# Kernel optimization log

Measured on AMD Instinct MI355X. Metric: run time of the kernel, lower is better.

Reference implementation:

```python
import jax, jax.numpy as jnp
import numpy as np

L, C, H, FF = 12, 768, 12, 3072
DH = C // H
VOCAB = 30522
B, P, T = 64, 196, 40
PATCH_FLAT = 768  # 16*16*3
MAXP, MAXW = P + 1, T + 2


def _ln(x, w, b, eps):
    m = jnp.mean(x, axis=-1, keepdims=True)
    v = jnp.mean(jnp.square(x - m), axis=-1, keepdims=True)
    return (x - m) * jax.lax.rsqrt(v + eps) * w + b


def setup_inputs() -> dict:
    key = jax.random.key(0)
    ks = iter(jax.random.split(key, 40))
    s = 0.02
    rn = lambda shape: jax.random.normal(next(ks), shape, jnp.float32) * s
    return {
        'vis_in': jax.random.normal(next(ks), (B, P, PATCH_FLAT), jnp.float32),
        'txt_in': jax.random.randint(next(ks), (B, T), 0, VOCAB),
        'vis_mask': jnp.ones((B, P), jnp.int32),
        'txt_mask': jnp.ones((B, T), jnp.int32),
        'patch_w': rn((C, PATCH_FLAT)), 'patch_b': jnp.zeros((C,), jnp.float32),
        'w_embed': rn((VOCAB, C)),
        't_pos': rn((MAXW, C)),
        'v_pos': rn((1, MAXP, C)),
        'v_cls': rn((1, 1, C)),
        'v_mod': rn((1, 1, C)), 't_mod': rn((1, 1, C)),
        'vn_w': jnp.ones((C,), jnp.float32), 'vn_b': jnp.zeros((C,), jnp.float32),
        'tn_w': jnp.ones((C,), jnp.float32), 'tn_b': jnp.zeros((C,), jnp.float32),
        'qkv_w': rn((L, 3 * C, C)), 'qkv_b': jnp.zeros((L, 3 * C), jnp.float32),
        'proj_w': rn((L, C, C)), 'proj_b': jnp.zeros((L, C), jnp.float32),
        'n1_w': jnp.ones((L, C), jnp.float32), 'n1_b': jnp.zeros((L, C), jnp.float32),
        'n2_w': jnp.ones((L, C), jnp.float32), 'n2_b': jnp.zeros((L, C), jnp.float32),
        'fc1_w': rn((L, FF, C)), 'fc1_b': jnp.zeros((L, FF), jnp.float32),
        'fc2_w': rn((L, C, FF)), 'fc2_b': jnp.zeros((L, C), jnp.float32),
    }


def reference(vis_in, txt_in, vis_mask, txt_mask, patch_w, patch_b, w_embed, t_pos,
              v_pos, v_cls, v_mod, t_mod, vn_w, vn_b, tn_w, tn_b, qkv_w, qkv_b,
              proj_w, proj_b, n1_w, n1_b, n2_w, n2_b, fc1_w, fc1_b, fc2_w, fc2_b):
    Bsz = vis_in.shape[0]
    # patch projection and word embedding
    v_emb = vis_in @ patch_w.T + patch_b                      # [B, P, C]
    t_emb = w_embed[txt_in]                                    # [B, T, C]
    v_emb = jnp.concatenate([jnp.broadcast_to(v_cls, (Bsz, 1, C)), v_emb], axis=1)
    VL = v_emb.shape[1]                                        # P + 1
    v_emb = _ln(v_emb + v_pos[:, :VL] + v_mod, vn_w, vn_b, 1e-5)
    t_emb = _ln(t_emb + t_pos[:T] + t_mod, tn_w, tn_b, 1e-5)
    x = jnp.concatenate([t_emb, v_emb], axis=1)                # [B, N, C], N = T+1+P
    m = jnp.concatenate([txt_mask, jnp.ones((Bsz, 1), txt_mask.dtype), vis_mask], axis=-1)
    # pairwise mask: attn_mask[b,i,j] == 0 -> masked (broadcast over heads)
    masked = (m[:, None, :, None] * m[:, None, None, :]) == 0  # [B,1,N,N]
    scale = DH ** -0.5
    for l in range(L):
        h = _ln(x, n1_w[l], n1_b[l], 1e-6)
        qkv = (h @ qkv_w[l].T + qkv_b[l]).reshape(Bsz, -1, 3, H, DH)
        q = jnp.transpose(qkv[:, :, 0], (0, 2, 1, 3))          # [B,H,N,DH]
        k = jnp.transpose(qkv[:, :, 1], (0, 2, 1, 3))
        v = jnp.transpose(qkv[:, :, 2], (0, 2, 1, 3))
        attn = jnp.einsum('bhqd,bhkd->bhqk', q, k) * scale
        attn = jnp.where(masked, jnp.asarray(-1e30, attn.dtype), attn)
        attn = jax.nn.softmax(attn, axis=-1)
        o = jnp.einsum('bhqk,bhkd->bhqd', attn, v)
        o = jnp.transpose(o, (0, 2, 1, 3)).reshape(Bsz, -1, C)
        x = x + (o @ proj_w[l].T + proj_b[l])
        h2 = _ln(x, n2_w[l], n2_b[l], 1e-6)
        h2 = jax.nn.gelu(h2 @ fc1_w[l].T + fc1_b[l], approximate=False)
        x = x + (h2 @ fc2_w[l].T + fc2_b[l])
    return x
```

## Files before the change

kernel.cpp:

```cpp
#include <hip/hip_runtime.h>
#include <hip/hip_bf16.h>

using bf16 = __hip_bfloat16;
typedef __bf16 bfv8 __attribute__((ext_vector_type(8)));
typedef float f32x4 __attribute__((ext_vector_type(4)));

#define DEVI __device__ __forceinline__

constexpr int L_ = 12, C_ = 768, H_ = 12, FF_ = 3072, DH_ = 64;
constexpr int B_ = 64, P_ = 196, T_ = 40;
constexpr int N_ = T_ + 1 + P_;
constexpr int M_ = B_ * N_;
constexpr int MPAD = 15360;
constexpr int NKV = 256;
constexpr int BP_ = B_ * P_;

constexpr size_t OFF_X   = 0;
constexpr size_t SZ_X    = (size_t)MPAD * C_ * 4;
constexpr size_t OFF_H   = OFF_X + SZ_X;
constexpr size_t SZ_H    = (size_t)MPAD * C_ * 2;
constexpr size_t OFF_Q   = OFF_H + SZ_H;
constexpr size_t SZ_QKV1 = (size_t)B_ * H_ * NKV * DH_ * 2;
constexpr size_t OFF_K   = OFF_Q + SZ_QKV1;
constexpr size_t OFF_V   = OFF_K + SZ_QKV1;
constexpr size_t OFF_O   = OFF_V + SZ_QKV1;
constexpr size_t SZ_O    = SZ_H;
constexpr size_t OFF_FFH = OFF_O + SZ_O;
constexpr size_t SZ_FFH  = (size_t)MPAD * FF_ * 2;
constexpr size_t OFF_WB  = OFF_FFH + SZ_FFH;
constexpr size_t SZ_WB   = (size_t)(2304 + 768 + 3072 + 3072) * 768 * 2;
constexpr size_t WS_NEED = OFF_WB + SZ_WB;
constexpr size_t OFF_PTMP = OFF_FFH;
constexpr size_t OFF_VISB = OFF_FFH + (size_t)40 * 1024 * 1024;
constexpr size_t OFF_PWB  = OFF_WB;

DEVI void gld_lds16(const bf16* g, bf16* l) {
  __builtin_amdgcn_global_load_lds((__attribute__((address_space(1))) void*)(g),
                                   (__attribute__((address_space(3))) void*)(l), 16, 0, 0);
}

DEVI void swz_tiles(int bid, int G, int NTC, int& bm, int& bn) {
  const int qq = G >> 3, rr = G & 7;
  const int xcd = bid & 7, base = bid >> 3;
  const int lin = (xcd < rr ? xcd * (qq + 1) : rr * (qq + 1) + (xcd - rr) * qq) + base;
  bm = lin / NTC;
  bn = lin - bm * NTC;
}

DEVI uint packbf(float lo, float hi) {
  union { struct { bf16 x, y; } h; uint u; } r;
  r.h.x = __float2bfloat16(lo); r.h.y = __float2bfloat16(hi);
  return r.u;
}

DEVI float gelu_f(float v) {
  const float p = v * (1.5957691f + 0.07135481f * v * v) * 1.442695041f;
  const float d = exp2f(-p);
  return v / (1.f + d);
}

template <int EPI>
__global__ __launch_bounds__(512, 2) void gemm3s(
    const bf16* __restrict__ A, const bf16* __restrict__ W,
    const float* __restrict__ bias, float* __restrict__ outf,
    float* __restrict__ outf2, bf16* __restrict__ outb,
    bf16* __restrict__ qb, bf16* __restrict__ kb, bf16* __restrict__ vb,
    int Nout, int K, int Mvalid, int NTC) {
  extern __shared__ __align__(16) char lds[];
  constexpr int SLOT = 49152;
  constexpr int BOFF = 32768;

  const int tid = threadIdx.x, wid = tid >> 6, lane = tid & 63;
  const int wm = wid >> 1, wn = wid & 1;
  int bm, bn;
  swz_tiles(blockIdx.x, gridDim.x, NTC, bm, bn);
  const size_t arow0 = (size_t)bm * 256;
  const size_t brow0 = (size_t)bn * 128;

  const int xr = ((lane & 7) ^ (lane >> 3)) * 8;
  const size_t aoff0 = (arow0 + (size_t)wid * 32 + (lane >> 3)) * K + xr;
  const size_t boff0 = (brow0 + (size_t)wid * 16 + (lane >> 3)) * K + xr;

  f32x4 acc[4][4];
#pragma unroll
  for (int m = 0; m < 4; m++)
#pragma unroll
    for (int n = 0; n < 4; n++) acc[m][n] = (f32x4){0.f, 0.f, 0.f, 0.f};

  auto STAGE = [&](int t, int so) {
    char* slot = lds + so;
    const bf16* Ag = A + aoff0 + (size_t)t * 64;
#pragma unroll
    for (int i = 0; i < 4; i++)
      gld_lds16(Ag + (size_t)i * 8 * K, (bf16*)(slot + (wid * 32 + i * 8) * 128));
    const bf16* Wg = W + boff0 + (size_t)t * 64;
#pragma unroll
    for (int i = 0; i < 2; i++)
      gld_lds16(Wg + (size_t)i * 8 * K, (bf16*)(slot + BOFF + (wid * 16 + i * 8) * 128));
  };

  const int la = lane & 15, g = lane >> 4;
  auto COMPUTE = [&](int so) {
    const char* slot = lds + so;
#pragma unroll
    for (int ks = 0; ks < 2; ks++) {
      bfv8 bfr[4];
#pragma unroll
      for (int n = 0; n < 4; n++) {
        const int r = wn * 64 + n * 16 + la;
        bfr[n] = *(const bfv8*)(slot + BOFF + r * 128 + (((ks * 4 + g) ^ (r & 7)) * 16));
      }
#pragma unroll
      for (int m = 0; m < 4; m++) {
        const int r = wm * 64 + m * 16 + la;
        bfv8 af = *(const bfv8*)(slot + r * 128 + (((ks * 4 + g) ^ (r & 7)) * 16));
#pragma unroll
        for (int n = 0; n < 4; n++)
          acc[m][n] = __builtin_amdgcn_mfma_f32_16x16x32_bf16(af, bfr[n], acc[m][n], 0, 0, 0);
      }
    }
  };

  const int NT = K >> 6;
  STAGE(0, 0);
  STAGE(1, SLOT);
  int cs = 0, sp = 2 * SLOT;
  for (int t = 0; t < NT; ++t) {
    if (t + 2 < NT) {
      STAGE(t + 2, sp);
      sp = (sp == 2 * SLOT) ? 0 : sp + SLOT;
      asm volatile("s_waitcnt vmcnt(12)" ::: "memory");
    } else if (t + 1 < NT) {
      asm volatile("s_waitcnt vmcnt(6)" ::: "memory");
    } else {
      asm volatile("s_waitcnt vmcnt(0)" ::: "memory");
    }
    asm volatile("s_barrier" ::: "memory");
    COMPUTE(cs);
    cs = (cs == 2 * SLOT) ? 0 : cs + SLOT;
    asm volatile("s_barrier" ::: "memory");
  }

  const int row0 = (int)arow0 + wm * 64;
  const int col0 = (int)brow0 + wn * 64;
  float bv[4];
#pragma unroll
  for (int n = 0; n < 4; n++) bv[n] = bias[col0 + n * 16 + la];

  if constexpr (EPI == 0 || EPI == 2 || EPI == 4) {
#pragma unroll
    for (int n = 0; n < 4; n++) {
      const int colb = col0 + n * 16 + la;
#pragma unroll
      for (int m = 0; m < 4; m++)
#pragma unroll
        for (int j = 0; j < 4; j++) {
          const int row = row0 + m * 16 + g * 4 + j;
          const float v = acc[m][n][j] + bv[n];
          if constexpr (EPI == 0) outf[(size_t)row * Nout + colb] = v;
          else if constexpr (EPI == 2) outf[(size_t)row * Nout + colb] += v;
          else { if (row < Mvalid) outf2[(size_t)row * Nout + colb] = outf[(size_t)row * Nout + colb] + v; }
        }
    }
  } else if constexpr (EPI == 3) {
#pragma unroll
    for (int m = 0; m < 4; m++)
#pragma unroll
      for (int j = 0; j < 4; j++) {
        const int row = row0 + m * 16 + g * 4 + j;
#pragma unroll
        for (int n = 0; n < 4; n++) {
          const float v = gelu_f(acc[m][n][j] + bv[n]);
          const float p = __shfl_xor(v, 1);
          if (!(lane & 1))
            *(uint*)(outb + (size_t)row * Nout + col0 + n * 16 + la) = packbf(v, p);
        }
      }
  } else {
#pragma unroll
    for (int m = 0; m < 4; m++)
#pragma unroll
      for (int j = 0; j < 4; j++) {
        const int row = row0 + m * 16 + g * 4 + j;
        const bool ok = row < Mvalid;
        const int bI = row / N_;
        const int nI = row - bI * N_;
#pragma unroll
        for (int n = 0; n < 4; n++) {
          const int colb = col0 + n * 16 + la;
          const float v = acc[m][n][j] + bv[n];
          const float p = __shfl_xor(v, 1);
          if (ok && !(lane & 1)) {
            const int s = colb / C_;
            const int rem = colb - s * C_;
            const int hh = rem >> 6, dd = rem & 63;
            bf16* dst = (s == 0) ? qb : (s == 1) ? kb : vb;
            *(uint*)(dst + (((size_t)bI * H_ + hh) * NKV + nI) * DH_ + dd) = packbf(v, p);
          }
        }
      }
  }
}

__global__ __launch_bounds__(256) void conv_weights_k(
    const float* __restrict__ wq, const float* __restrict__ wp,
    const float* __restrict__ wf1, const float* __restrict__ wf2,
    bf16* __restrict__ dst) {
  const long n0 = 2304L * 768 / 4, n1 = 768L * 768 / 4;
  const long n2 = 3072L * 768 / 4;
  const long tot = n0 + n1 + 2 * n2;
  for (long i = (long)blockIdx.x * 256 + threadIdx.x; i < tot; i += (long)gridDim.x * 256) {
    const float* s; long off;
    if (i < n0) { s = wq; off = i; }
    else if (i < n0 + n1) { s = wp; off = i - n0; }
    else if (i < n0 + n1 + n2) { s = wf1; off = i - n0 - n1; }
    else { s = wf2; off = i - n0 - n1 - n2; }
    float4 v = ((const float4*)s)[off];
    union { short4 q; bf16 h[4]; } u;
    u.h[0] = __float2bfloat16(v.x); u.h[1] = __float2bfloat16(v.y);
    u.h[2] = __float2bfloat16(v.z); u.h[3] = __float2bfloat16(v.w);
    ((short4*)dst)[i] = u.q;
  }
}

__global__ __launch_bounds__(256) void f32_to_bf16_k(const float* __restrict__ s,
                                                     bf16* __restrict__ d, long n4) {
  long i = (long)blockIdx.x * 256 + threadIdx.x;
  long stride = (long)gridDim.x * 256;
  for (; i < n4; i += stride) {
    float4 v = ((const float4*)s)[i];
    union { short4 q; bf16 h[4]; } u;
    u.h[0] = __float2bfloat16(v.x); u.h[1] = __float2bfloat16(v.y);
    u.h[2] = __float2bfloat16(v.z); u.h[3] = __float2bfloat16(v.w);
    ((short4*)d)[i] = u.q;
  }
}

__global__ __launch_bounds__(256) void embed_kernel(
    const float* __restrict__ ptmp, const int* __restrict__ txt_in,
    const float* __restrict__ wemb, const float* __restrict__ tpos,
    const float* __restrict__ vpos, const float* __restrict__ vcls,
    const float* __restrict__ vmod, const float* __restrict__ tmod,
    const float* __restrict__ vnw, const float* __restrict__ vnb,
    const float* __restrict__ tnw, const float* __restrict__ tnb,
    float* __restrict__ x) {
  const int row = blockIdx.x;
  const int tid = threadIdx.x;
  if (row >= M_) {
    for (int i = tid; i < C_; i += 256) x[(size_t)row * C_ + i] = 0.f;
    return;
  }
  const int b = row / N_, n = row - (row / N_) * N_;
  const bool istxt = n < T_;
  float e[3];
#pragma unroll
  for (int i = 0; i < 3; i++) {
    const int c = tid + i * 256;
    float v;
    if (istxt) {
      v = wemb[(size_t)txt_in[b * T_ + n] * C_ + c] + tpos[n * C_ + c] + tmod[c];
    } else {
      const int vi = n - T_;
      const float base = (vi == 0) ? vcls[c] : ptmp[((size_t)b * P_ + (vi - 1)) * C_ + c];
      v = base + vpos[vi * C_ + c] + vmod[c];
    }
    e[i] = v;
  }
  float s = e[0] + e[1] + e[2];
  float s2 = e[0] * e[0] + e[1] * e[1] + e[2] * e[2];
#pragma unroll
  for (int d = 1; d < 64; d <<= 1) { s += __shfl_xor(s, d); s2 += __shfl_xor(s2, d); }
  __shared__ float rs[4], rs2[4];
  const int wid = tid >> 6, lane = tid & 63;
  if (lane == 0) { rs[wid] = s; rs2[wid] = s2; }
  __syncthreads();
  s = rs[0] + rs[1] + rs[2] + rs[3];
  s2 = rs2[0] + rs2[1] + rs2[2] + rs2[3];
  const float mean = s * (1.f / C_);
  const float var = s2 * (1.f / C_) - mean * mean;
  const float rr = rsqrtf(var + 1e-5f);
  const float* w = istxt ? tnw : vnw;
  const float* bb = istxt ? tnb : vnb;
#pragma unroll
  for (int i = 0; i < 3; i++) {
    const int c = tid + i * 256;
    x[(size_t)row * C_ + c] = (e[i] - mean) * rr * w[c] + bb[c];
  }
}

__global__ __launch_bounds__(256) void ln_rows(const float* __restrict__ x,
                                               const float* __restrict__ w,
                                               const float* __restrict__ b,
                                               bf16* __restrict__ out, float eps) {
  const int row = blockIdx.x * 4 + (threadIdx.x >> 6);
  const int lane = threadIdx.x & 63;
  if (row >= MPAD) return;
  bf16* op = out + (size_t)row * C_;
  if (row >= M_) {
#pragma unroll
    for (int i = 0; i < 3; i++)
      *(short4*)(op + (lane + 64 * i) * 4) = make_short4(0, 0, 0, 0);
    return;
  }
  const float4* xp = (const float4*)(x + (size_t)row * C_);
  float4 v[3];
  float s = 0.f, s2 = 0.f;
#pragma unroll
  for (int i = 0; i < 3; i++) {
    v[i] = xp[lane + 64 * i];
    s += v[i].x + v[i].y + v[i].z + v[i].w;
    s2 += v[i].x * v[i].x + v[i].y * v[i].y + v[i].z * v[i].z + v[i].w * v[i].w;
  }
#pragma unroll
  for (int d = 1; d < 64; d <<= 1) { s += __shfl_xor(s, d); s2 += __shfl_xor(s2, d); }
  const float mean = s * (1.f / C_);
  const float rr = rsqrtf(s2 * (1.f / C_) - mean * mean + eps);
#pragma unroll
  for (int i = 0; i < 3; i++) {
    const int c0 = (lane + 64 * i) * 4;
    const float4 w4 = *(const float4*)(w + c0);
    const float4 b4 = *(const float4*)(b + c0);
    union { short4 s4; bf16 h[4]; } u;
    u.h[0] = __float2bfloat16((v[i].x - mean) * rr * w4.x + b4.x);
    u.h[1] = __float2bfloat16((v[i].y - mean) * rr * w4.y + b4.y);
    u.h[2] = __float2bfloat16((v[i].z - mean) * rr * w4.z + b4.z);
    u.h[3] = __float2bfloat16((v[i].w - mean) * rr * w4.w + b4.w);
    *(short4*)(op + c0) = u.s4;
  }
}

DEVI float maskval(const int* __restrict__ tm, const int* __restrict__ vm, int b, int j) {
  if (j < T_) return tm[b * T_ + j] ? 1.f : 0.f;
  if (j == T_) return 1.f;
  if (j < N_) return vm[b * P_ + (j - T_ - 1)] ? 1.f : 0.f;
  return 0.f;
}

__global__ __launch_bounds__(256) void attn_fused(
    const bf16* __restrict__ qb, const bf16* __restrict__ kb,
    const bf16* __restrict__ vb, const int* __restrict__ txt_mask,
    const int* __restrict__ vis_mask, bf16* __restrict__ ob) {
  __shared__ alignas(16) __bf16 Vt[64 * 264];
  __shared__ alignas(16) __bf16 Ps[64 * 264];
  const int qblk = blockIdx.x;
  const int bh = blockIdx.y;
  const int b = bh / H_, hh = bh - b * H_;
  const int tid = threadIdx.x, wid = tid >> 6, lane = tid & 63;

  const __bf16* Vg = (const __bf16*)(vb + (size_t)bh * NKV * DH_);
#pragma unroll
  for (int it = 0; it < 8; it++) {
    const int r = lane + 64 * (it & 3);
    const int c8 = (wid + 4 * (it >> 2)) * 8;
    bfv8 v;
    if (r < N_) v = *(const bfv8*)(Vg + (size_t)r * DH_ + c8);
    else { union { int4 i; bfv8 x; } z; z.i = make_int4(0,0,0,0); v = z.x; }
#pragma unroll
    for (int d = 0; d < 8; d++) Vt[(c8 + d) * 264 + r] = v[d];
  }

  const int qbase = qblk * 64 + wid * 16;
  const __bf16* Qg = (const __bf16*)(qb + (size_t)bh * NKV * DH_);
  const __bf16* Kg = (const __bf16*)(kb + (size_t)bh * NKV * DH_);
  bfv8 aq[2];
#pragma unroll
  for (int kk = 0; kk < 2; kk++)
    aq[kk] = *(const bfv8*)(Qg + (size_t)(qbase + (lane & 15)) * DH_ + kk * 32 + (lane >> 4) * 8);

  f32x4 acc[16];
#pragma unroll
  for (int f = 0; f < 16; f++) acc[f] = (f32x4){0.f, 0.f, 0.f, 0.f};
#pragma unroll
  for (int f = 0; f < 16; f++) {
#pragma unroll
    for (int kk = 0; kk < 2; kk++) {
      bfv8 bk = *(const bfv8*)(Kg + (size_t)(f * 16 + (lane & 15)) * DH_ + kk * 32 + (lane >> 4) * 8);
      acc[f] = __builtin_amdgcn_mfma_f32_16x16x32_bf16(aq[kk], bk, acc[f], 0, 0, 0);
    }
  }

  float cm[16];
#pragma unroll
  for (int f = 0; f < 16; f++)
    cm[f] = maskval(txt_mask, vis_mask, b, f * 16 + (lane & 15));

  const float scale = 0.125f;
#pragma unroll
  for (int j = 0; j < 4; j++) {
    const int qr = qbase + (lane >> 4) * 4 + j;
    const float qm = (qr < N_) ? maskval(txt_mask, vis_mask, b, qr) : 1.f;
    float sv[16];
    float mx = -3.0e38f;
#pragma unroll
    for (int f = 0; f < 16; f++) {
      const int col = f * 16 + (lane & 15);
      float sc;
      if (col >= N_) sc = -INFINITY;
      else if (qm * cm[f] == 0.f) sc = -1e30f;
      else sc = acc[f][j] * scale;
      sv[f] = sc;
      mx = fmaxf(mx, sc);
    }
#pragma unroll
    for (int d = 1; d < 16; d <<= 1) mx = fmaxf(mx, __shfl_xor(mx, d));
    float sum = 0.f;
#pragma unroll
    for (int f = 0; f < 16; f++) { const float p = expf(sv[f] - mx); sv[f] = p; sum += p; }
#pragma unroll
    for (int d = 1; d < 16; d <<= 1) sum += __shfl_xor(sum, d);
    const float inv = 1.f / sum;
    const int ql = wid * 16 + (lane >> 4) * 4 + j;
#pragma unroll
    for (int f = 0; f < 16; f++)
      Ps[ql * 264 + f * 16 + (lane & 15)] = (__bf16)(sv[f] * inv);
  }

  __syncthreads();

  f32x4 oacc[4];
#pragma unroll
  for (int n = 0; n < 4; n++) oacc[n] = (f32x4){0.f, 0.f, 0.f, 0.f};
#pragma unroll
  for (int kk = 0; kk < 8; kk++) {
    bfv8 ap = *(const bfv8*)&Ps[(wid * 16 + (lane & 15)) * 264 + kk * 32 + (lane >> 4) * 8];
#pragma unroll
    for (int n = 0; n < 4; n++) {
      bfv8 bv = *(const bfv8*)&Vt[(n * 16 + (lane & 15)) * 264 + kk * 32 + (lane >> 4) * 8];
      oacc[n] = __builtin_amdgcn_mfma_f32_16x16x32_bf16(ap, bv, oacc[n], 0, 0, 0);
    }
  }
#pragma unroll
  for (int n = 0; n < 4; n++)
#pragma unroll
    for (int j = 0; j < 4; j++) {
      const int q = qbase + (lane >> 4) * 4 + j;
      if (q < N_)
        ob[((size_t)b * N_ + q) * C_ + hh * 64 + n * 16 + (lane & 15)] =
            __float2bfloat16(oacc[n][j]);
    }
}

extern "C" void kernel_launch(void* const* d_in, const int* in_sizes, int n_in,
                              void* d_out, int out_size, void* d_ws, size_t ws_size,
                              hipStream_t stream) {
  const float* vis_in  = (const float*)d_in[0];
  const int*   txt_in  = (const int*)d_in[1];
  const int*   vis_mask = (const int*)d_in[2];
  const int*   txt_mask = (const int*)d_in[3];
  const float* patch_w = (const float*)d_in[4];
  const float* patch_b = (const float*)d_in[5];
  const float* w_embed = (const float*)d_in[6];
  const float* t_pos   = (const float*)d_in[7];
  const float* v_pos   = (const float*)d_in[8];
  const float* v_cls   = (const float*)d_in[9];
  const float* v_mod   = (const float*)d_in[10];
  const float* t_mod   = (const float*)d_in[11];
  const float* vn_w = (const float*)d_in[12];
  const float* vn_b = (const float*)d_in[13];
  const float* tn_w = (const float*)d_in[14];
  const float* tn_b = (const float*)d_in[15];
  const float* qkv_w = (const float*)d_in[16];
  const float* qkv_b = (const float*)d_in[17];
  const float* proj_w = (const float*)d_in[18];
  const float* proj_b = (const float*)d_in[19];
  const float* n1_w = (const float*)d_in[20];
  const float* n1_b = (const float*)d_in[21];
  const float* n2_w = (const float*)d_in[22];
  const float* n2_b = (const float*)d_in[23];
  const float* fc1_w = (const float*)d_in[24];
  const float* fc1_b = (const float*)d_in[25];
  const float* fc2_w = (const float*)d_in[26];
  const float* fc2_b = (const float*)d_in[27];

  char* ws = (char*)d_ws;
  if (ws_size < WS_NEED) {
    hipMemsetAsync(d_out, 0, (size_t)out_size * 4, stream);
    return;
  }
  float* x    = (float*)(ws + OFF_X);
  bf16* h     = (bf16*)(ws + OFF_H);
  bf16* qbuf  = (bf16*)(ws + OFF_Q);
  bf16* kbuf  = (bf16*)(ws + OFF_K);
  bf16* vbuf  = (bf16*)(ws + OFF_V);
  bf16* obuf  = (bf16*)(ws + OFF_O);
  bf16* ffh   = (bf16*)(ws + OFF_FFH);
  bf16* wq    = (bf16*)(ws + OFF_WB);
  bf16* wp    = wq + (size_t)2304 * 768;
  bf16* wf1   = wp + (size_t)768 * 768;
  bf16* wf2   = wf1 + (size_t)3072 * 768;
  float* ptmp = (float*)(ws + OFF_PTMP);
  bf16* visb  = (bf16*)(ws + OFF_VISB);
  bf16* pwb   = (bf16*)(ws + OFF_PWB);

  constexpr int LDS3 = 3 * 49152;
  (void)hipFuncSetAttribute((const void*)gemm3s<0>, hipFuncAttributeMaxDynamicSharedMemorySize, LDS3);
  (void)hipFuncSetAttribute((const void*)gemm3s<1>, hipFuncAttributeMaxDynamicSharedMemorySize, LDS3);
  (void)hipFuncSetAttribute((const void*)gemm3s<2>, hipFuncAttributeMaxDynamicSharedMemorySize, LDS3);
  (void)hipFuncSetAttribute((const void*)gemm3s<3>, hipFuncAttributeMaxDynamicSharedMemorySize, LDS3);
  (void)hipFuncSetAttribute((const void*)gemm3s<4>, hipFuncAttributeMaxDynamicSharedMemorySize, LDS3);

  f32_to_bf16_k<<<1024, 256, 0, stream>>>(vis_in, visb, (long)BP_ * C_ / 4);
  f32_to_bf16_k<<<256, 256, 0, stream>>>(patch_w, pwb, (long)C_ * C_ / 4);
  gemm3s<0><<<(BP_ / 256) * (C_ / 128), 512, LDS3, stream>>>(
      visb, pwb, patch_b, ptmp, nullptr, nullptr, nullptr, nullptr, nullptr,
      C_, C_, BP_, C_ / 128);
  embed_kernel<<<MPAD, 256, 0, stream>>>(ptmp, txt_in, w_embed, t_pos, v_pos, v_cls,
                                         v_mod, t_mod, vn_w, vn_b, tn_w, tn_b, x);

  for (int l = 0; l < L_; l++) {
    conv_weights_k<<<2048, 256, 0, stream>>>(
        qkv_w + (size_t)l * 2304 * 768, proj_w + (size_t)l * 768 * 768,
        fc1_w + (size_t)l * 3072 * 768, fc2_w + (size_t)l * 768 * 3072, wq);

    ln_rows<<<MPAD / 4, 256, 0, stream>>>(x, n1_w + l * C_, n1_b + l * C_, h, 1e-6f);
    gemm3s<1><<<(MPAD / 256) * (2304 / 128), 512, LDS3, stream>>>(
        h, wq, qkv_b + (size_t)l * 2304, nullptr, nullptr, nullptr, qbuf, kbuf, vbuf,
        2304, C_, M_, 2304 / 128);
    attn_fused<<<dim3(4, B_ * H_), 256, 0, stream>>>(qbuf, kbuf, vbuf, txt_mask,
                                                     vis_mask, obuf);
    gemm3s<2><<<(MPAD / 256) * (C_ / 128), 512, LDS3, stream>>>(
        obuf, wp, proj_b + (size_t)l * C_, x, nullptr, nullptr, nullptr, nullptr,
        nullptr, C_, C_, M_, C_ / 128);
    ln_rows<<<MPAD / 4, 256, 0, stream>>>(x, n2_w + l * C_, n2_b + l * C_, h, 1e-6f);
    gemm3s<3><<<(MPAD / 256) * (FF_ / 128), 512, LDS3, stream>>>(
        h, wf1, fc1_b + (size_t)l * FF_, nullptr, nullptr, ffh, nullptr, nullptr,
        nullptr, FF_, C_, M_, FF_ / 128);
    if (l < L_ - 1) {
      gemm3s<2><<<(MPAD / 256) * (C_ / 128), 512, LDS3, stream>>>(
          ffh, wf2, fc2_b + (size_t)l * C_, x, nullptr, nullptr, nullptr, nullptr,
          nullptr, C_, FF_, M_, C_ / 128);
    } else {
      gemm3s<4><<<(MPAD / 256) * (C_ / 128), 512, LDS3, stream>>>(
          ffh, wf2, fc2_b + (size_t)l * C_, x, (float*)d_out, nullptr, nullptr,
          nullptr, nullptr, C_, FF_, M_, C_ / 128);
    }
  }
}
```

Baseline: 6.728 ms.

## Restructure GEMM main loop into interleaved two-phase load/MFMA schedule with priority

The GEMM inner loop is split into two half-phases. Each phase loads its LDS fragments into registers, issues part of the next tile's global-to-LDS prefetch, then runs a batch of MFMAs under raised wave priority (s_setprio). The intent is to interleave memory traffic with matrix math across waves, in the style of ping-pong scheduling, rather than staging a whole tile and then computing. Launch bounds drop to one block per CU, which frees registers for the preloaded A fragments but gives up the possibility of two resident blocks. Three LDS slots of 48KB each already exceed what two blocks could share, so occupancy may be unchanged in practice.

```diff
diff --git a/kernel.cpp b/kernel.cpp
--- a/kernel.cpp
+++ b/kernel.cpp
@@ -60,7 +60,7 @@
 }
 
 template <int EPI>
-__global__ __launch_bounds__(512, 2) void gemm3s(
+__global__ __launch_bounds__(512, 1) void gemm8p(
     const bf16* __restrict__ A, const bf16* __restrict__ W,
     const float* __restrict__ bias, float* __restrict__ outf,
     float* __restrict__ outf2, bf16* __restrict__ outb,
@@ -87,58 +87,91 @@
 #pragma unroll
     for (int n = 0; n < 4; n++) acc[m][n] = (f32x4){0.f, 0.f, 0.f, 0.f};
 
-  auto STAGE = [&](int t, int so) {
-    char* slot = lds + so;
+  auto STGa = [&](int t, int so) {
     const bf16* Ag = A + aoff0 + (size_t)t * 64;
-#pragma unroll
-    for (int i = 0; i < 4; i++)
-      gld_lds16(Ag + (size_t)i * 8 * K, (bf16*)(slot + (wid * 32 + i * 8) * 128));
+    char* s = lds + so;
+#pragma unroll
+    for (int i = 0; i < 3; i++)
+      gld_lds16(Ag + (size_t)i * 8 * K, (bf16*)(s + (wid * 32 + i * 8) * 128));
+  };
+  auto STGb = [&](int t, int so) {
+    const bf16* Ag = A + aoff0 + (size_t)t * 64;
     const bf16* Wg = W + boff0 + (size_t)t * 64;
+    char* s = lds + so;
+    gld_lds16(Ag + (size_t)24 * K, (bf16*)(s + (wid * 32 + 24) * 128));
 #pragma unroll
     for (int i = 0; i < 2; i++)
-      gld_lds16(Wg + (size_t)i * 8 * K, (bf16*)(slot + BOFF + (wid * 16 + i * 8) * 128));
+      gld_lds16(Wg + (size_t)i * 8 * K, (bf16*)(s + BOFF + (wid * 16 + i * 8) * 128));
   };
 
   const int la = lane & 15, g = lane >> 4;
-  auto COMPUTE = [&](int so) {
-    const char* slot = lds + so;
-#pragma unroll
-    for (int ks = 0; ks < 2; ks++) {
-      bfv8 bfr[4];
-#pragma unroll
-      for (int n = 0; n < 4; n++) {
+
+  const int NT = K >> 6;
+  STGa(0, 0); STGb(0, 0);
+  STGa(1, SLOT); STGb(1, SLOT);
+  asm volatile("s_waitcnt vmcnt(6)" ::: "memory");
+  __builtin_amdgcn_s_barrier();
+
+  int cs = 0;
+  for (int t = 0; t < NT; ++t) {
+    const int so = cs;
+    int sn = cs + 2 * SLOT; if (sn >= 3 * SLOT) sn -= 3 * SLOT;
+    const char* sa = lds + so;
+    const bool pf = (t + 2 < NT);
+
+    bfv8 af[8], bf0[4];
+#pragma unroll
+    for (int m = 0; m < 4; m++)
+#pragma unroll
+      for (int ks = 0; ks < 2; ks++) {
+        const int r = wm * 64 + m * 16 + la;
+        af[m * 2 + ks] = *(const bfv8*)(sa + r * 128 + (((ks * 4 + g) ^ (r & 7)) * 16));
+      }
+#pragma unroll
+    for (int n = 0; n < 2; n++)
+#pragma unroll
+      for (int ks = 0; ks < 2; ks++) {
         const int r = wn * 64 + n * 16 + la;
-        bfr[n] = *(const bfv8*)(slot + BOFF + r * 128 + (((ks * 4 + g) ^ (r & 7)) * 16));
+        bf0[n * 2 + ks] = *(const bfv8*)(sa + BOFF + r * 128 + (((ks * 4 + g) ^ (r & 7)) * 16));
       }
-#pragma unroll
-      for (int m = 0; m < 4; m++) {
-        const int r = wm * 64 + m * 16 + la;
-        bfv8 af = *(const bfv8*)(slot + r * 128 + (((ks * 4 + g) ^ (r & 7)) * 16));
-#pragma unroll
-        for (int n = 0; n < 4; n++)
-          acc[m][n] = __builtin_amdgcn_mfma_f32_16x16x32_bf16(af, bfr[n], acc[m][n], 0, 0, 0);
+    if (pf) STGa(t + 2, sn);
+    __builtin_amdgcn_s_barrier();
+    __builtin_amdgcn_s_setprio(1);
+#pragma unroll
+    for (int ks = 0; ks < 2; ks++)
+#pragma unroll
+      for (int m = 0; m < 4; m++)
+#pragma unroll
+        for (int n = 0; n < 2; n++)
+          acc[m][n] = __builtin_amdgcn_mfma_f32_16x16x32_bf16(af[m * 2 + ks], bf0[n * 2 + ks],
+                                                              acc[m][n], 0, 0, 0);
+    __builtin_amdgcn_s_setprio(0);
+
+    bfv8 bf1[4];
+#pragma unroll
+    for (int n = 0; n < 2; n++)
+#pragma unroll
+      for (int ks = 0; ks < 2; ks++) {
+        const int r = wn * 64 + (n + 2) * 16 + la;
+        bf1[n * 2 + ks] = *(const bfv8*)(sa + BOFF + r * 128 + (((ks * 4 + g) ^ (r & 7)) * 16));
       }
-    }
-  };
-
-  const int NT = K >> 6;
-  STAGE(0, 0);
-  STAGE(1, SLOT);
-  int cs = 0, sp = 2 * SLOT;
-  for (int t = 0; t < NT; ++t) {
-    if (t + 2 < NT) {
-      STAGE(t + 2, sp);
-      sp = (sp == 2 * SLOT) ? 0 : sp + SLOT;
-      asm volatile("s_waitcnt vmcnt(12)" ::: "memory");
-    } else if (t + 1 < NT) {
-      asm volatile("s_waitcnt vmcnt(6)" ::: "memory");
-    } else {
-      asm volatile("s_waitcnt vmcnt(0)" ::: "memory");
-    }
-    asm volatile("s_barrier" ::: "memory");
-    COMPUTE(cs);
+    if (pf) STGb(t + 2, sn);
+    __builtin_amdgcn_s_barrier();
+    __builtin_amdgcn_s_setprio(1);
+#pragma unroll
+    for (int ks = 0; ks < 2; ks++)
+#pragma unroll
+      for (int m = 0; m < 4; m++)
+#pragma unroll
+        for (int n = 0; n < 2; n++)
+          acc[m][n + 2] = __builtin_amdgcn_mfma_f32_16x16x32_bf16(af[m * 2 + ks], bf1[n * 2 + ks],
+                                                                  acc[m][n + 2], 0, 0, 0);
+    __builtin_amdgcn_s_setprio(0);
+
+    if (pf) asm volatile("s_waitcnt vmcnt(6)" ::: "memory");
+    else    asm volatile("s_waitcnt vmcnt(0)" ::: "memory");
+    __builtin_amdgcn_s_barrier();
     cs = (cs == 2 * SLOT) ? 0 : cs + SLOT;
-    asm volatile("s_barrier" ::: "memory");
   }
 
   const int row0 = (int)arow0 + wm * 64;
@@ -493,15 +526,15 @@
   bf16* pwb   = (bf16*)(ws + OFF_PWB);
 
   constexpr int LDS3 = 3 * 49152;
-  (void)hipFuncSetAttribute((const void*)gemm3s<0>, hipFuncAttributeMaxDynamicSharedMemorySize, LDS3);
-  (void)hipFuncSetAttribute((const void*)gemm3s<1>, hipFuncAttributeMaxDynamicSharedMemorySize, LDS3);
-  (void)hipFuncSetAttribute((const void*)gemm3s<2>, hipFuncAttributeMaxDynamicSharedMemorySize, LDS3);
-  (void)hipFuncSetAttribute((const void*)gemm3s<3>, hipFuncAttributeMaxDynamicSharedMemorySize, LDS3);
-  (void)hipFuncSetAttribute((const void*)gemm3s<4>, hipFuncAttributeMaxDynamicSharedMemorySize, LDS3);
+  (void)hipFuncSetAttribute((const void*)gemm8p<0>, hipFuncAttributeMaxDynamicSharedMemorySize, LDS3);
+  (void)hipFuncSetAttribute((const void*)gemm8p<1>, hipFuncAttributeMaxDynamicSharedMemorySize, LDS3);
+  (void)hipFuncSetAttribute((const void*)gemm8p<2>, hipFuncAttributeMaxDynamicSharedMemorySize, LDS3);
+  (void)hipFuncSetAttribute((const void*)gemm8p<3>, hipFuncAttributeMaxDynamicSharedMemorySize, LDS3);
+  (void)hipFuncSetAttribute((const void*)gemm8p<4>, hipFuncAttributeMaxDynamicSharedMemorySize, LDS3);
 
   f32_to_bf16_k<<<1024, 256, 0, stream>>>(vis_in, visb, (long)BP_ * C_ / 4);
   f32_to_bf16_k<<<256, 256, 0, stream>>>(patch_w, pwb, (long)C_ * C_ / 4);
-  gemm3s<0><<<(BP_ / 256) * (C_ / 128), 512, LDS3, stream>>>(
+  gemm8p<0><<<(BP_ / 256) * (C_ / 128), 512, LDS3, stream>>>(
       visb, pwb, patch_b, ptmp, nullptr, nullptr, nullptr, nullptr, nullptr,
       C_, C_, BP_, C_ / 128);
   embed_kernel<<<MPAD, 256, 0, stream>>>(ptmp, txt_in, w_embed, t_pos, v_pos, v_cls,
@@ -513,24 +546,24 @@
         fc1_w + (size_t)l * 3072 * 768, fc2_w + (size_t)l * 768 * 3072, wq);
 
     ln_rows<<<MPAD / 4, 256, 0, stream>>>(x, n1_w + l * C_, n1_b + l * C_, h, 1e-6f);
-    gemm3s<1><<<(MPAD / 256) * (2304 / 128), 512, LDS3, stream>>>(
+    gemm8p<1><<<(MPAD / 256) * (2304 / 128), 512, LDS3, stream>>>(
         h, wq, qkv_b + (size_t)l * 2304, nullptr, nullptr, nullptr, qbuf, kbuf, vbuf,
         2304, C_, M_, 2304 / 128);
     attn_fused<<<dim3(4, B_ * H_), 256, 0, stream>>>(qbuf, kbuf, vbuf, txt_mask,
                                                      vis_mask, obuf);
-    gemm3s<2><<<(MPAD / 256) * (C_ / 128), 512, LDS3, stream>>>(
+    gemm8p<2><<<(MPAD / 256) * (C_ / 128), 512, LDS3, stream>>>(
         obuf, wp, proj_b + (size_t)l * C_, x, nullptr, nullptr, nullptr, nullptr,
         nullptr, C_, C_, M_, C_ / 128);
     ln_rows<<<MPAD / 4, 256, 0, stream>>>(x, n2_w + l * C_, n2_b + l * C_, h, 1e-6f);
-    gemm3s<3><<<(MPAD / 256) * (FF_ / 128), 512, LDS3, stream>>>(
+    gemm8p<3><<<(MPAD / 256) * (FF_ / 128), 512, LDS3, stream>>>(
         h, wf1, fc1_b + (size_t)l * FF_, nullptr, nullptr, ffh, nullptr, nullptr,
         nullptr, FF_, C_, M_, FF_ / 128);
     if (l < L_ - 1) {
-      gemm3s<2><<<(MPAD / 256) * (C_ / 128), 512, LDS3, stream>>>(
+      gemm8p<2><<<(MPAD / 256) * (C_ / 128), 512, LDS3, stream>>>(
           ffh, wf2, fc2_b + (size_t)l * C_, x, nullptr, nullptr, nullptr, nullptr,
           nullptr, C_, FF_, M_, C_ / 128);
     } else {
-      gemm3s<4><<<(MPAD / 256) * (C_ / 128), 512, LDS3, stream>>>(
+      gemm8p<4><<<(MPAD / 256) * (C_ / 128), 512, LDS3, stream>>>(
           ffh, wf2, fc2_b + (size_t)l * C_, x, (float*)d_out, nullptr, nullptr,
           nullptr, nullptr, C_, FF_, M_, C_ / 128);
     }
```

New measurement: 6.694 ms. No clear change (-0.5%).

## Replace 256x128 triple-buffered GEMM with 128x128 double-buffered static-LDS kernel

Applied to the files above, without the earlier changes.

The GEMM kernel used a 256x128 output tile with 512 threads, K-step 64, and three 48KB dynamic LDS slots. It is replaced by a 128x128 tile with 256 threads, K-step 32, and two small static LDS buffers using a rotated-chunk swizzle. The aim is to cut LDS footprint and raise occupancy while doubling the block count for better CU load balance. The cost is less operand reuse per tile, shallower prefetch and twice as many barriers per unit of K.

```diff
diff --git a/kernel.cpp b/kernel.cpp
--- a/kernel.cpp
+++ b/kernel.cpp
@@ -60,26 +60,40 @@
 }
 
 template <int EPI>
-__global__ __launch_bounds__(512, 2) void gemm3s(
+__global__ __launch_bounds__(256) void gemm_mb(
     const bf16* __restrict__ A, const bf16* __restrict__ W,
     const float* __restrict__ bias, float* __restrict__ outf,
     float* __restrict__ outf2, bf16* __restrict__ outb,
     bf16* __restrict__ qb, bf16* __restrict__ kb, bf16* __restrict__ vb,
     int Nout, int K, int Mvalid, int NTC) {
-  extern __shared__ __align__(16) char lds[];
-  constexpr int SLOT = 49152;
-  constexpr int BOFF = 32768;
+  __shared__ alignas(16) bf16 As[2][128 * 32];
+  __shared__ alignas(16) bf16 Bs[2][128 * 32];
 
   const int tid = threadIdx.x, wid = tid >> 6, lane = tid & 63;
   const int wm = wid >> 1, wn = wid & 1;
   int bm, bn;
   swz_tiles(blockIdx.x, gridDim.x, NTC, bm, bn);
-  const size_t arow0 = (size_t)bm * 256;
+  const size_t arow0 = (size_t)bm * 128;
   const size_t brow0 = (size_t)bn * 128;
 
-  const int xr = ((lane & 7) ^ (lane >> 3)) * 8;
-  const size_t aoff0 = (arow0 + (size_t)wid * 32 + (lane >> 3)) * K + xr;
-  const size_t boff0 = (brow0 + (size_t)wid * 16 + (lane >> 3)) * K + xr;
+  const int srow = tid >> 2;
+  const int gch = ((tid & 3) - ((tid >> 3) & 3)) & 3;
+  const bf16* pa0 = A + (arow0 + srow) * K + gch * 8;
+  const bf16* pa1 = A + (arow0 + 64 + srow) * K + gch * 8;
+  const bf16* pb0 = W + (brow0 + srow) * K + gch * 8;
+  const bf16* pb1 = W + (brow0 + 64 + srow) * K + gch * 8;
+  bf16* da0[2] = {&As[0][(wid * 16) * 32], &As[1][(wid * 16) * 32]};
+  bf16* da1[2] = {&As[0][(64 + wid * 16) * 32], &As[1][(64 + wid * 16) * 32]};
+  bf16* db0[2] = {&Bs[0][(wid * 16) * 32], &Bs[1][(wid * 16) * 32]};
+  bf16* db1[2] = {&Bs[0][(64 + wid * 16) * 32], &Bs[1][(64 + wid * 16) * 32]};
+
+  auto STAGE = [&](int t, int b) {
+    const size_t k = (size_t)t * 32;
+    gld_lds16(pa0 + k, da0[b]);
+    gld_lds16(pa1 + k, da1[b]);
+    gld_lds16(pb0 + k, db0[b]);
+    gld_lds16(pb1 + k, db1[b]);
+  };
 
   f32x4 acc[4][4];
 #pragma unroll
@@ -87,57 +101,32 @@
 #pragma unroll
     for (int n = 0; n < 4; n++) acc[m][n] = (f32x4){0.f, 0.f, 0.f, 0.f};
 
-  auto STAGE = [&](int t, int so) {
-    char* slot = lds + so;
-    const bf16* Ag = A + aoff0 + (size_t)t * 64;
-#pragma unroll
-    for (int i = 0; i < 4; i++)
-      gld_lds16(Ag + (size_t)i * 8 * K, (bf16*)(slot + (wid * 32 + i * 8) * 128));
-    const bf16* Wg = W + boff0 + (size_t)t * 64;
-#pragma unroll
-    for (int i = 0; i < 2; i++)
-      gld_lds16(Wg + (size_t)i * 8 * K, (bf16*)(slot + BOFF + (wid * 16 + i * 8) * 128));
-  };
-
   const int la = lane & 15, g = lane >> 4;
-  auto COMPUTE = [&](int so) {
-    const char* slot = lds + so;
-#pragma unroll
-    for (int ks = 0; ks < 2; ks++) {
-      bfv8 bfr[4];
-#pragma unroll
-      for (int n = 0; n < 4; n++) {
-        const int r = wn * 64 + n * 16 + la;
-        bfr[n] = *(const bfv8*)(slot + BOFF + r * 128 + (((ks * 4 + g) ^ (r & 7)) * 16));
-      }
-#pragma unroll
-      for (int m = 0; m < 4; m++) {
-        const int r = wm * 64 + m * 16 + la;
-        bfv8 af = *(const bfv8*)(slot + r * 128 + (((ks * 4 + g) ^ (r & 7)) * 16));
-#pragma unroll
-        for (int n = 0; n < 4; n++)
-          acc[m][n] = __builtin_amdgcn_mfma_f32_16x16x32_bf16(af, bfr[n], acc[m][n], 0, 0, 0);
-      }
-    }
-  };
-
-  const int NT = K >> 6;
+  const int slot8 = ((g + (la >> 1)) & 3) * 8;
+
+  const int NT = K >> 5;
   STAGE(0, 0);
-  STAGE(1, SLOT);
-  int cs = 0, sp = 2 * SLOT;
   for (int t = 0; t < NT; ++t) {
-    if (t + 2 < NT) {
-      STAGE(t + 2, sp);
-      sp = (sp == 2 * SLOT) ? 0 : sp + SLOT;
-      asm volatile("s_waitcnt vmcnt(12)" ::: "memory");
-    } else if (t + 1 < NT) {
-      asm volatile("s_waitcnt vmcnt(6)" ::: "memory");
+    const int b = t & 1;
+    if (t + 1 < NT) {
+      STAGE(t + 1, b ^ 1);
+      asm volatile("s_waitcnt vmcnt(4)" ::: "memory");
     } else {
       asm volatile("s_waitcnt vmcnt(0)" ::: "memory");
     }
     asm volatile("s_barrier" ::: "memory");
-    COMPUTE(cs);
-    cs = (cs == 2 * SLOT) ? 0 : cs + SLOT;
+    bfv8 af[4], bfr[4];
+#pragma unroll
+    for (int n = 0; n < 4; n++)
+      bfr[n] = *(const bfv8*)&Bs[b][(wn * 64 + n * 16 + la) * 32 + slot8];
+#pragma unroll
+    for (int m = 0; m < 4; m++)
+      af[m] = *(const bfv8*)&As[b][(wm * 64 + m * 16 + la) * 32 + slot8];
+#pragma unroll
+    for (int m = 0; m < 4; m++)
+#pragma unroll
+      for (int n = 0; n < 4; n++)
+        acc[m][n] = __builtin_amdgcn_mfma_f32_16x16x32_bf16(af[m], bfr[n], acc[m][n], 0, 0, 0);
     asm volatile("s_barrier" ::: "memory");
   }
 
@@ -492,16 +481,9 @@
   bf16* visb  = (bf16*)(ws + OFF_VISB);
   bf16* pwb   = (bf16*)(ws + OFF_PWB);
 
-  constexpr int LDS3 = 3 * 49152;
-  (void)hipFuncSetAttribute((const void*)gemm3s<0>, hipFuncAttributeMaxDynamicSharedMemorySize, LDS3);
-  (void)hipFuncSetAttribute((const void*)gemm3s<1>, hipFuncAttributeMaxDynamicSharedMemorySize, LDS3);
-  (void)hipFuncSetAttribute((const void*)gemm3s<2>, hipFuncAttributeMaxDynamicSharedMemorySize, LDS3);
-  (void)hipFuncSetAttribute((const void*)gemm3s<3>, hipFuncAttributeMaxDynamicSharedMemorySize, LDS3);
-  (void)hipFuncSetAttribute((const void*)gemm3s<4>, hipFuncAttributeMaxDynamicSharedMemorySize, LDS3);
-
   f32_to_bf16_k<<<1024, 256, 0, stream>>>(vis_in, visb, (long)BP_ * C_ / 4);
   f32_to_bf16_k<<<256, 256, 0, stream>>>(patch_w, pwb, (long)C_ * C_ / 4);
-  gemm3s<0><<<(BP_ / 256) * (C_ / 128), 512, LDS3, stream>>>(
+  gemm_mb<0><<<(BP_ / 128) * (C_ / 128), 256, 0, stream>>>(
       visb, pwb, patch_b, ptmp, nullptr, nullptr, nullptr, nullptr, nullptr,
       C_, C_, BP_, C_ / 128);
   embed_kernel<<<MPAD, 256, 0, stream>>>(ptmp, txt_in, w_embed, t_pos, v_pos, v_cls,
@@ -513,24 +495,24 @@
         fc1_w + (size_t)l * 3072 * 768, fc2_w + (size_t)l * 768 * 3072, wq);
 
     ln_rows<<<MPAD / 4, 256, 0, stream>>>(x, n1_w + l * C_, n1_b + l * C_, h, 1e-6f);
-    gemm3s<1><<<(MPAD / 256) * (2304 / 128), 512, LDS3, stream>>>(
+    gemm_mb<1><<<(MPAD / 128) * (2304 / 128), 256, 0, stream>>>(
         h, wq, qkv_b + (size_t)l * 2304, nullptr, nullptr, nullptr, qbuf, kbuf, vbuf,
         2304, C_, M_, 2304 / 128);
     attn_fused<<<dim3(4, B_ * H_), 256, 0, stream>>>(qbuf, kbuf, vbuf, txt_mask,
                                                      vis_mask, obuf);
-    gemm3s<2><<<(MPAD / 256) * (C_ / 128), 512, LDS3, stream>>>(
+    gemm_mb<2><<<(MPAD / 128) * (C_ / 128), 256, 0, stream>>>(
         obuf, wp, proj_b + (size_t)l * C_, x, nullptr, nullptr, nullptr, nullptr,
         nullptr, C_, C_, M_, C_ / 128);
     ln_rows<<<MPAD / 4, 256, 0, stream>>>(x, n2_w + l * C_, n2_b + l * C_, h, 1e-6f);
-    gemm3s<3><<<(MPAD / 256) * (FF_ / 128), 512, LDS3, stream>>>(
+    gemm_mb<3><<<(MPAD / 128) * (FF_ / 128), 256, 0, stream>>>(
         h, wf1, fc1_b + (size_t)l * FF_, nullptr, nullptr, ffh, nullptr, nullptr,
         nullptr, FF_, C_, M_, FF_ / 128);
     if (l < L_ - 1) {
-      gemm3s<2><<<(MPAD / 256) * (C_ / 128), 512, LDS3, stream>>>(
+      gemm_mb<2><<<(MPAD / 128) * (C_ / 128), 256, 0, stream>>>(
           ffh, wf2, fc2_b + (size_t)l * C_, x, nullptr, nullptr, nullptr, nullptr,
           nullptr, C_, FF_, M_, C_ / 128);
     } else {
-      gemm3s<4><<<(MPAD / 256) * (C_ / 128), 512, LDS3, stream>>>(
+      gemm_mb<4><<<(MPAD / 128) * (C_ / 128), 256, 0, stream>>>(
           ffh, wf2, fc2_b + (size_t)l * C_, x, (float*)d_out, nullptr, nullptr,
           nullptr, nullptr, C_, FF_, M_, C_ / 128);
     }
```

New measurement: 6.019 ms. -10.5%, faster.
